# Optimization experiments

Measured on AMD Instinct MI355X. Metric: run time of the kernel, lower is better.

## Reference

```python
import jax, jax.numpy as jnp
import numpy as np

D_MODEL, D_K, D_V = 512, 64, 64
LN_EPS = 1e-6


def setup_inputs() -> dict:
    key = jax.random.key(0)
    ks = jax.random.split(key, 8)
    B, Lq, Lk = 2, 1024, 1024
    q = jax.random.normal(ks[0], (B, Lq, D_MODEL), dtype=jnp.float32)
    k = jax.random.normal(ks[1], (B, Lk, D_MODEL), dtype=jnp.float32)
    v = jax.random.normal(ks[2], (B, Lk, D_MODEL), dtype=jnp.float32)
    s = 1.0 / np.sqrt(D_MODEL)
    Wq = jax.random.normal(ks[3], (D_MODEL, D_K), dtype=jnp.float32) * s
    Wk = jax.random.normal(ks[4], (D_MODEL, D_K), dtype=jnp.float32) * s
    Wv = jax.random.normal(ks[5], (D_MODEL, D_V), dtype=jnp.float32) * s
    v_param = jax.random.normal(ks[6], (D_K,), dtype=jnp.float32)
    Wfc = jax.random.normal(ks[7], (D_V, D_MODEL), dtype=jnp.float32) / np.sqrt(D_V)
    ln_gamma = jnp.ones((D_MODEL,), dtype=jnp.float32)
    ln_beta = jnp.zeros((D_MODEL,), dtype=jnp.float32)
    return {"q": q, "k": k, "v": v, "Wq": Wq, "Wk": Wk, "Wv": Wv,
            "v_param": v_param, "Wfc": Wfc, "ln_gamma": ln_gamma, "ln_beta": ln_beta}


def reference(q, k, v, Wq, Wk, Wv, v_param, Wfc, ln_gamma, ln_beta):
    residual = q
    qp = q @ Wq                      # [B, Lq, d_k]
    kp = k @ Wk                      # [B, Lk, d_k]
    vp = v @ Wv                      # [B, Lk, d_v]
    # additive (Bahdanau) scores: tanh(q_i + k_j) . v_param  -> [B, Lq, Lk]
    scores = jnp.einsum("bqkd,d->bqk", jnp.tanh(qp[:, :, None, :] + kp[:, None, :, :]), v_param)
    attn = jax.nn.softmax(scores, axis=-1)   # dropout is identity in eval mode
    out = jnp.einsum("bqk,bkv->bqv", attn, vp)
    out = out @ Wfc + residual               # [B, Lq, d_model]
    mu = jnp.mean(out, axis=-1, keepdims=True)
    var = jnp.var(out, axis=-1, keepdims=True)
    out = (out - mu) * jax.lax.rsqrt(var + LN_EPS) * ln_gamma + ln_beta
    return out, attn
```

## Files before the change

### kernel.cpp

```cpp
#include <hip/hip_runtime.h>
#include <cstddef>
#include <cstdint>

#define D_MODEL 512
#define DK 64
#define LQ 1024
#define LK 1024
#define NB 2
#define LN_EPS 1e-6f
#define L2E2 2.8853900817779268f

__device__ __forceinline__ uint32_t pack_bf2(float a, float b) {
  uint32_t ua = __float_as_uint(a), ub = __float_as_uint(b);
  ua = (ua + 0x7fffu + ((ua >> 16) & 1u)) >> 16;
  ub = (ub + 0x7fffu + ((ub >> 16) & 1u)) >> 16;
  return (ub << 16) | ua;
}

#define PR_ROWS 8
__global__ __launch_bounds__(256, 4) void proj_kernel(
    const float* __restrict__ q, const float* __restrict__ k,
    const float* __restrict__ v, const float* __restrict__ Wq,
    const float* __restrict__ Wk, const float* __restrict__ Wv,
    const float* __restrict__ v_param, float2* __restrict__ ab_g,
    uint32_t* __restrict__ ekT, float* __restrict__ vp) {
  __shared__ float rows[PR_ROWS][D_MODEL];
  const int tid = threadIdx.x;
  const int type = blockIdx.x >> 8;
  const int r0 = (blockIdx.x & 255) * PR_ROWS;
  const float* __restrict__ in = (type == 0) ? q : (type == 1) ? k : v;
  const float* __restrict__ W = (type == 0) ? Wq : (type == 1) ? Wk : Wv;
  {
    const float4* __restrict__ in4 = (const float4*)(in + (size_t)r0 * D_MODEL);
    float4* r4 = (float4*)&rows[0][0];
#pragma unroll
    for (int t = 0; t < 4; ++t) r4[tid + 256 * t] = in4[tid + 256 * t];
  }
  __syncthreads();
  const int lane = tid & 63;
  const int wv = tid >> 6;
  const int rglob = r0 + wv * 2;
  const float* __restrict__ Wl = W + lane;
  const float* __restrict__ rA = rows[wv * 2];
  const float* __restrict__ rB = rows[wv * 2 + 1];
  float c0a = 0.f, c1a = 0.f, c0b = 0.f, c1b = 0.f;
#pragma unroll 2
  for (int e = 0; e < D_MODEL; e += 4) {
    float w0 = Wl[(size_t)(e + 0) * DK];
    float w1 = Wl[(size_t)(e + 1) * DK];
    float w2 = Wl[(size_t)(e + 2) * DK];
    float w3 = Wl[(size_t)(e + 3) * DK];
    float4 xa = *(const float4*)&rA[e];
    float4 xb = *(const float4*)&rB[e];
    c0a = fmaf(xa.x, w0, c0a); c1a = fmaf(xa.y, w1, c1a);
    c0a = fmaf(xa.z, w2, c0a); c1a = fmaf(xa.w, w3, c1a);
    c0b = fmaf(xb.x, w0, c0b); c1b = fmaf(xb.y, w1, c1b);
    c0b = fmaf(xb.z, w2, c0b); c1b = fmaf(xb.w, w3, c1b);
  }
  float acc0 = c0a + c1a, acc1 = c0b + c1b;
  if (type == 0) {
    float vpar = v_param[lane];
    float i0 = __builtin_amdgcn_exp2f(-L2E2 * acc0);
    float i1 = __builtin_amdgcn_exp2f(-L2E2 * acc1);
    ab_g[(size_t)(rglob + 0) * DK + lane] = make_float2(vpar * i0, i0);
    ab_g[(size_t)(rglob + 1) * DK + lane] = make_float2(vpar * i1, i1);
  } else if (type == 1) {
    float e0 = __builtin_amdgcn_exp2f(L2E2 * acc0);
    float e1 = __builtin_amdgcn_exp2f(L2E2 * acc1);
    float h0 = __shfl_down(e0, 32);
    float h1 = __shfl_down(e1, 32);
    if (lane < 32) {
      int b = rglob >> 10, j0 = rglob & 1023;
      uint2 pk;
      pk.x = pack_bf2(e0, h0);
      pk.y = pack_bf2(e1, h1);
      *(uint2*)&ekT[(size_t)b * 32 * LK + (size_t)lane * LK + j0] = pk;
    }
  } else {
    vp[(size_t)(rglob + 0) * DK + lane] = acc0;
    vp[(size_t)(rglob + 1) * DK + lane] = acc1;
  }
}

#define RB 2
__global__ __launch_bounds__(256, 4) void score_kernel(
    const float2* __restrict__ ab_g, const uint32_t* __restrict__ ekT,
    float* __restrict__ attn_out) {
  __shared__ float4 ab4s[RB][32];
  __shared__ float mred[RB][4], sred[RB][4];
  const int tid = threadIdx.x;
  const int row0 = blockIdx.x * RB;
  const int batch = row0 >> 10;
  const uint32_t* __restrict__ ekT_b = ekT + (size_t)batch * 32 * LK;
  if (tid < RB * 64) {
    int r = tid >> 6, d = tid & 63;
    float2 abv = ab_g[(size_t)(row0 + r) * DK + d];
    ((float2*)&ab4s[r][d & 31])[d >> 5] = abv;
  }
  __syncthreads();

  float acc[RB][4];
#pragma unroll
  for (int r = 0; r < RB; ++r)
#pragma unroll
    for (int jj = 0; jj < 4; ++jj) acc[r][jj] = 0.f;

#pragma unroll 2
  for (int dp = 0; dp < 32; ++dp) {
    float klo[4], khi[4];
#pragma unroll
    for (int jj = 0; jj < 4; ++jj) {
      uint32_t kw = ekT_b[(size_t)dp * LK + tid + jj * 256];
      klo[jj] = __uint_as_float(kw << 16);
      khi[jj] = __uint_as_float(kw & 0xffff0000u);
    }
#pragma unroll
    for (int r = 0; r < RB; ++r) {
      float4 ab = ab4s[r][dp];
#pragma unroll
      for (int jj = 0; jj < 4; ++jj) {
        float x1 = klo[jj] + ab.y, x2 = khi[jj] + ab.w;
        float num = fmaf(ab.z, x1, ab.x * x2);
        acc[r][jj] = fmaf(num, __builtin_amdgcn_rcpf(x1 * x2), acc[r][jj]);
      }
    }
  }

  const int wave = __builtin_amdgcn_readfirstlane(tid >> 6);
  const int lane = tid & 63;

  {
#pragma unroll
    for (int r = 0; r < RB; ++r) {
      float pm = fminf(fminf(acc[r][0], acc[r][1]), fminf(acc[r][2], acc[r][3]));
#pragma unroll
      for (int off = 32; off > 0; off >>= 1) pm = fminf(pm, __shfl_xor(pm, off));
      if (lane == 0) mred[r][wave] = pm;
    }
    __syncthreads();
#pragma unroll
    for (int r = 0; r < RB; ++r) {
      float m = fminf(fminf(mred[r][0], mred[r][1]),
                      fminf(mred[r][2], mred[r][3]));
      float s = 0.f;
#pragma unroll
      for (int jj = 0; jj < 4; ++jj) {
        float e = __builtin_amdgcn_exp2f((m - acc[r][jj]) * L2E2);
        acc[r][jj] = e;
        s += e;
      }
#pragma unroll
      for (int off = 32; off > 0; off >>= 1) s += __shfl_xor(s, off);
      if (lane == 0) sred[r][wave] = s;
    }
    __syncthreads();
#pragma unroll
    for (int r = 0; r < RB; ++r) {
      float inv = __builtin_amdgcn_rcpf(sred[r][0] + sred[r][1] + sred[r][2] +
                                        sred[r][3]);
      float* __restrict__ arow = attn_out + (size_t)(row0 + r) * LK;
#pragma unroll
      for (int jj = 0; jj < 4; ++jj)
        arow[tid + jj * 256] = acc[r][jj] * inv;
    }
  }
}

#define PRB 4
__global__ __launch_bounds__(512, 4) void pvfc_kernel(
    const float* __restrict__ attn, const float* __restrict__ vp,
    const float* __restrict__ resid, const float* __restrict__ Wfc,
    const float* __restrict__ gamma, const float* __restrict__ beta,
    float* __restrict__ out) {
  __shared__ float sc[PRB][LK];
  __shared__ float4 pvred[8][PRB][16];
  __shared__ __align__(16) float ovlT[DK][PRB];
  __shared__ float red[2][PRB][8];
  const int tid = threadIdx.x;
  const int row0 = blockIdx.x * PRB;
  const int batch = row0 >> 10;
  const float* __restrict__ vp_b = vp + (size_t)batch * LK * DK;
  {
    const float4* __restrict__ a4 = (const float4*)(attn + (size_t)row0 * LK);
    float4* s4 = (float4*)&sc[0][0];
#pragma unroll
    for (int t = 0; t < 2; ++t) s4[tid + 512 * t] = a4[tid + 512 * t];
  }
  __syncthreads();

  const int wave = __builtin_amdgcn_readfirstlane(tid >> 6);
  const int lane = tid & 63;

  {
    const int jj = lane >> 4, l16 = lane & 15;
    const float4* __restrict__ vp4 = (const float4*)vp_b;
    float4 a[PRB];
#pragma unroll
    for (int r = 0; r < PRB; ++r) a[r] = make_float4(0.f, 0.f, 0.f, 0.f);
#pragma unroll 4
    for (int it = 0; it < 32; ++it) {
      int j = (wave << 7) + (it << 2) + jj;
      float4 vv = vp4[(size_t)j * (DK / 4) + l16];
#pragma unroll
      for (int r = 0; r < PRB; ++r) {
        float pw = sc[r][j];
        a[r].x = fmaf(pw, vv.x, a[r].x);
        a[r].y = fmaf(pw, vv.y, a[r].y);
        a[r].z = fmaf(pw, vv.z, a[r].z);
        a[r].w = fmaf(pw, vv.w, a[r].w);
      }
    }
#pragma unroll
    for (int r = 0; r < PRB; ++r) {
      a[r].x += __shfl_xor(a[r].x, 16); a[r].y += __shfl_xor(a[r].y, 16);
      a[r].z += __shfl_xor(a[r].z, 16); a[r].w += __shfl_xor(a[r].w, 16);
      a[r].x += __shfl_xor(a[r].x, 32); a[r].y += __shfl_xor(a[r].y, 32);
      a[r].z += __shfl_xor(a[r].z, 32); a[r].w += __shfl_xor(a[r].w, 32);
    }
    if (jj == 0) {
#pragma unroll
      for (int r = 0; r < PRB; ++r) pvred[wave][r][l16] = a[r];
    }
  }
  __syncthreads();
  if (tid < 64) {
    int r = tid >> 4, l16 = tid & 15;
    float4 s = make_float4(0.f, 0.f, 0.f, 0.f);
#pragma unroll
    for (int w = 0; w < 8; ++w) {
      float4 t = pvred[w][r][l16];
      s.x += t.x; s.y += t.y; s.z += t.z; s.w += t.w;
    }
    ovlT[l16 * 4 + 0][r] = s.x;
    ovlT[l16 * 4 + 1][r] = s.y;
    ovlT[l16 * 4 + 2][r] = s.z;
    ovlT[l16 * 4 + 3][r] = s.w;
  }
  __syncthreads();

  {
    const int c = tid;
    float y[PRB];
#pragma unroll
    for (int r = 0; r < PRB; ++r)
      y[r] = resid[(size_t)(row0 + r) * D_MODEL + c];
#pragma unroll 4
    for (int e = 0; e < DK; ++e) {
      float w = Wfc[(size_t)e * D_MODEL + c];
      float4 ov = *(const float4*)&ovlT[e][0];
      y[0] = fmaf(ov.x, w, y[0]);
      y[1] = fmaf(ov.y, w, y[1]);
      y[2] = fmaf(ov.z, w, y[2]);
      y[3] = fmaf(ov.w, w, y[3]);
    }
#pragma unroll
    for (int r = 0; r < PRB; ++r) {
      float s = y[r];
#pragma unroll
      for (int off = 32; off > 0; off >>= 1) s += __shfl_xor(s, off);
      if (lane == 0) red[0][r][wave] = s;
    }
    __syncthreads();
    float mu[PRB];
#pragma unroll
    for (int r = 0; r < PRB; ++r) {
      float s = 0.f;
#pragma unroll
      for (int w = 0; w < 8; ++w) s += red[0][r][w];
      mu[r] = s * (1.0f / D_MODEL);
    }
#pragma unroll
    for (int r = 0; r < PRB; ++r) {
      float d = y[r] - mu[r];
      float s = d * d;
#pragma unroll
      for (int off = 32; off > 0; off >>= 1) s += __shfl_xor(s, off);
      if (lane == 0) red[1][r][wave] = s;
    }
    __syncthreads();
    float gg = gamma[c], bb = beta[c];
#pragma unroll
    for (int r = 0; r < PRB; ++r) {
      float s = 0.f;
#pragma unroll
      for (int w = 0; w < 8; ++w) s += red[1][r][w];
      float var = s * (1.0f / D_MODEL);
      float rstd = rsqrtf(var + LN_EPS);
      out[(size_t)(row0 + r) * D_MODEL + c] = (y[r] - mu[r]) * rstd * gg + bb;
    }
  }
}

extern "C" void kernel_launch(void* const* d_in, const int* in_sizes, int n_in,
                              void* d_out, int out_size, void* d_ws,
                              size_t ws_size, hipStream_t stream) {
  const float* q = (const float*)d_in[0];
  const float* k = (const float*)d_in[1];
  const float* v = (const float*)d_in[2];
  const float* Wq = (const float*)d_in[3];
  const float* Wk = (const float*)d_in[4];
  const float* Wv = (const float*)d_in[5];
  const float* v_param = (const float*)d_in[6];
  const float* Wfc = (const float*)d_in[7];
  const float* gamma = (const float*)d_in[8];
  const float* beta = (const float*)d_in[9];

  float* out = (float*)d_out;
  float* attn = out + (size_t)NB * LQ * D_MODEL;

  float* base = (float*)d_ws;
  float2* ab_g = (float2*)base;
  uint32_t* ekT = (uint32_t*)(base + (size_t)2 * NB * LQ * DK);
  float* vp = base + (size_t)2 * NB * LQ * DK + NB * 32 * LK;

  hipLaunchKernelGGL(proj_kernel, dim3(3 * 256), dim3(256), 0, stream, q, k, v,
                     Wq, Wk, Wv, v_param, ab_g, ekT, vp);
  hipLaunchKernelGGL(score_kernel, dim3(NB * LQ / RB), dim3(256), 0, stream,
                     ab_g, ekT, attn);
  hipLaunchKernelGGL(pvfc_kernel, dim3(NB * LQ / PRB), dim3(512), 0, stream,
                     attn, vp, q, Wfc, gamma, beta, out);
}
```

Before: 65.29 us.

## Double-buffer key loads in score kernel and widen projection row tile

The score kernel's loop over the 32 packed key dimensions now uses two register buffers: the next group of 4 dimensions is loaded while the current group is computed. This is meant to hide global-load latency behind the rcp/FMA work. Separately, the projection kernel handles 16 rows per block (4 per wave) instead of 8, so each loaded weight value is reused across more rows and fewer blocks are launched. The trade-off is higher register pressure in both kernels and less block-level parallelism in the projection.

```diff
diff --git a/kernel.cpp b/kernel.cpp
--- a/kernel.cpp
+++ b/kernel.cpp
@@ -17,7 +17,7 @@
   return (ub << 16) | ua;
 }
 
-#define PR_ROWS 8
+#define PR_ROWS 16
 __global__ __launch_bounds__(256, 4) void proj_kernel(
     const float* __restrict__ q, const float* __restrict__ k,
     const float* __restrict__ v, const float* __restrict__ Wq,
@@ -26,59 +26,66 @@
     uint32_t* __restrict__ ekT, float* __restrict__ vp) {
   __shared__ float rows[PR_ROWS][D_MODEL];
   const int tid = threadIdx.x;
-  const int type = blockIdx.x >> 8;
-  const int r0 = (blockIdx.x & 255) * PR_ROWS;
+  const int type = blockIdx.x >> 7;
+  const int r0 = (blockIdx.x & 127) * PR_ROWS;
   const float* __restrict__ in = (type == 0) ? q : (type == 1) ? k : v;
   const float* __restrict__ W = (type == 0) ? Wq : (type == 1) ? Wk : Wv;
   {
     const float4* __restrict__ in4 = (const float4*)(in + (size_t)r0 * D_MODEL);
     float4* r4 = (float4*)&rows[0][0];
 #pragma unroll
-    for (int t = 0; t < 4; ++t) r4[tid + 256 * t] = in4[tid + 256 * t];
+    for (int t = 0; t < 8; ++t) r4[tid + 256 * t] = in4[tid + 256 * t];
   }
   __syncthreads();
   const int lane = tid & 63;
   const int wv = tid >> 6;
-  const int rglob = r0 + wv * 2;
+  const int rglob = r0 + wv * 4;
   const float* __restrict__ Wl = W + lane;
-  const float* __restrict__ rA = rows[wv * 2];
-  const float* __restrict__ rB = rows[wv * 2 + 1];
-  float c0a = 0.f, c1a = 0.f, c0b = 0.f, c1b = 0.f;
+  float c0[4] = {0.f, 0.f, 0.f, 0.f}, c1[4] = {0.f, 0.f, 0.f, 0.f};
 #pragma unroll 2
   for (int e = 0; e < D_MODEL; e += 4) {
     float w0 = Wl[(size_t)(e + 0) * DK];
     float w1 = Wl[(size_t)(e + 1) * DK];
     float w2 = Wl[(size_t)(e + 2) * DK];
     float w3 = Wl[(size_t)(e + 3) * DK];
-    float4 xa = *(const float4*)&rA[e];
-    float4 xb = *(const float4*)&rB[e];
-    c0a = fmaf(xa.x, w0, c0a); c1a = fmaf(xa.y, w1, c1a);
-    c0a = fmaf(xa.z, w2, c0a); c1a = fmaf(xa.w, w3, c1a);
-    c0b = fmaf(xb.x, w0, c0b); c1b = fmaf(xb.y, w1, c1b);
-    c0b = fmaf(xb.z, w2, c0b); c1b = fmaf(xb.w, w3, c1b);
-  }
-  float acc0 = c0a + c1a, acc1 = c0b + c1b;
+#pragma unroll
+    for (int r = 0; r < 4; ++r) {
+      float4 x = *(const float4*)&rows[wv * 4 + r][e];
+      c0[r] = fmaf(x.x, w0, c0[r]);
+      c1[r] = fmaf(x.y, w1, c1[r]);
+      c0[r] = fmaf(x.z, w2, c0[r]);
+      c1[r] = fmaf(x.w, w3, c1[r]);
+    }
+  }
+  float acc[4];
+#pragma unroll
+  for (int r = 0; r < 4; ++r) acc[r] = c0[r] + c1[r];
   if (type == 0) {
     float vpar = v_param[lane];
-    float i0 = __builtin_amdgcn_exp2f(-L2E2 * acc0);
-    float i1 = __builtin_amdgcn_exp2f(-L2E2 * acc1);
-    ab_g[(size_t)(rglob + 0) * DK + lane] = make_float2(vpar * i0, i0);
-    ab_g[(size_t)(rglob + 1) * DK + lane] = make_float2(vpar * i1, i1);
+#pragma unroll
+    for (int r = 0; r < 4; ++r) {
+      float iv = __builtin_amdgcn_exp2f(-L2E2 * acc[r]);
+      ab_g[(size_t)(rglob + r) * DK + lane] = make_float2(vpar * iv, iv);
+    }
   } else if (type == 1) {
-    float e0 = __builtin_amdgcn_exp2f(L2E2 * acc0);
-    float e1 = __builtin_amdgcn_exp2f(L2E2 * acc1);
-    float h0 = __shfl_down(e0, 32);
-    float h1 = __shfl_down(e1, 32);
+    float e4[4], h4[4];
+#pragma unroll
+    for (int r = 0; r < 4; ++r) {
+      e4[r] = __builtin_amdgcn_exp2f(L2E2 * acc[r]);
+      h4[r] = __shfl_down(e4[r], 32);
+    }
     if (lane < 32) {
       int b = rglob >> 10, j0 = rglob & 1023;
-      uint2 pk;
-      pk.x = pack_bf2(e0, h0);
-      pk.y = pack_bf2(e1, h1);
-      *(uint2*)&ekT[(size_t)b * 32 * LK + (size_t)lane * LK + j0] = pk;
+      uint4 pk;
+      pk.x = pack_bf2(e4[0], h4[0]);
+      pk.y = pack_bf2(e4[1], h4[1]);
+      pk.z = pack_bf2(e4[2], h4[2]);
+      pk.w = pack_bf2(e4[3], h4[3]);
+      *(uint4*)&ekT[(size_t)b * 32 * LK + (size_t)lane * LK + j0] = pk;
     }
   } else {
-    vp[(size_t)(rglob + 0) * DK + lane] = acc0;
-    vp[(size_t)(rglob + 1) * DK + lane] = acc1;
+#pragma unroll
+    for (int r = 0; r < 4; ++r) vp[(size_t)(rglob + r) * DK + lane] = acc[r];
   }
 }
 
@@ -91,7 +98,7 @@
   const int tid = threadIdx.x;
   const int row0 = blockIdx.x * RB;
   const int batch = row0 >> 10;
-  const uint32_t* __restrict__ ekT_b = ekT + (size_t)batch * 32 * LK;
+  const uint32_t* __restrict__ ekT_b = ekT + (size_t)batch * 32 * LK + tid;
   if (tid < RB * 64) {
     int r = tid >> 6, d = tid & 63;
     float2 abv = ab_g[(size_t)(row0 + r) * DK + d];
@@ -105,26 +112,48 @@
 #pragma unroll
     for (int jj = 0; jj < 4; ++jj) acc[r][jj] = 0.f;
 
-#pragma unroll 2
-  for (int dp = 0; dp < 32; ++dp) {
-    float klo[4], khi[4];
-#pragma unroll
-    for (int jj = 0; jj < 4; ++jj) {
-      uint32_t kw = ekT_b[(size_t)dp * LK + tid + jj * 256];
-      klo[jj] = __uint_as_float(kw << 16);
-      khi[jj] = __uint_as_float(kw & 0xffff0000u);
-    }
-#pragma unroll
-    for (int r = 0; r < RB; ++r) {
-      float4 ab = ab4s[r][dp];
-#pragma unroll
-      for (int jj = 0; jj < 4; ++jj) {
-        float x1 = klo[jj] + ab.y, x2 = khi[jj] + ab.w;
-        float num = fmaf(ab.z, x1, ab.x * x2);
-        acc[r][jj] = fmaf(num, __builtin_amdgcn_rcpf(x1 * x2), acc[r][jj]);
-      }
-    }
-  }
+  uint32_t bufA[4][4], bufB[4][4];
+
+#define PREF(BUF, TP)                                                      \
+  {                                                                        \
+    _Pragma("unroll") for (int dd = 0; dd < 4; ++dd) {                     \
+      _Pragma("unroll") for (int jj = 0; jj < 4; ++jj) {                   \
+        BUF[dd][jj] = ekT_b[(size_t)((TP)*4 + dd) * LK + jj * 256];        \
+      }                                                                    \
+    }                                                                      \
+  }
+
+#define COMP(BUF, TP)                                                      \
+  {                                                                        \
+    _Pragma("unroll") for (int dd = 0; dd < 4; ++dd) {                     \
+      const int dp = (TP)*4 + dd;                                          \
+      float klo[4], khi[4];                                                \
+      _Pragma("unroll") for (int jj = 0; jj < 4; ++jj) {                   \
+        klo[jj] = __uint_as_float(BUF[dd][jj] << 16);                      \
+        khi[jj] = __uint_as_float(BUF[dd][jj] & 0xffff0000u);              \
+      }                                                                    \
+      _Pragma("unroll") for (int r = 0; r < RB; ++r) {                     \
+        float4 ab = ab4s[r][dp];                                           \
+        _Pragma("unroll") for (int jj = 0; jj < 4; ++jj) {                 \
+          float x1 = klo[jj] + ab.y, x2 = khi[jj] + ab.w;                  \
+          float num = fmaf(ab.z, x1, ab.x * x2);                           \
+          acc[r][jj] =                                                     \
+              fmaf(num, __builtin_amdgcn_rcpf(x1 * x2), acc[r][jj]);       \
+        }                                                                  \
+      }                                                                    \
+    }                                                                      \
+  }
+
+  PREF(bufA, 0);
+#pragma unroll
+  for (int tp = 0; tp < 8; tp += 2) {
+    PREF(bufB, tp + 1);
+    COMP(bufA, tp);
+    if (tp + 2 < 8) PREF(bufA, tp + 2);
+    COMP(bufB, tp + 1);
+  }
+#undef PREF
+#undef COMP
 
   const int wave = __builtin_amdgcn_readfirstlane(tid >> 6);
   const int lane = tid & 63;
@@ -313,7 +342,7 @@
   uint32_t* ekT = (uint32_t*)(base + (size_t)2 * NB * LQ * DK);
   float* vp = base + (size_t)2 * NB * LQ * DK + NB * 32 * LK;
 
-  hipLaunchKernelGGL(proj_kernel, dim3(3 * 256), dim3(256), 0, stream, q, k, v,
+  hipLaunchKernelGGL(proj_kernel, dim3(3 * 128), dim3(256), 0, stream, q, k, v,
                      Wq, Wk, Wv, v_param, ab_g, ekT, vp);
   hipLaunchKernelGGL(score_kernel, dim3(NB * LQ / RB), dim3(256), 0, stream,
                      ab_g, ekT, attn);
```

Result: slower. 223.3 us (+241.9%).
